# Kernel tuning notes

Measured on AMD Instinct MI355X. Metric: run time of the kernel, lower is better.

## Reference

```python
import jax, jax.numpy as jnp
from jax import lax
import numpy as np

CHI, CHO = 256, 256
B, H, W = 4, 64, 64
KH = KW = 3
K = KH * KW
EPS = 1e-5


def setup_inputs() -> dict:
    key = jax.random.key(0)
    ks = jax.random.split(key, 8)
    x = jax.random.normal(ks[0], (B, CHI, H, W), jnp.float32)
    # offset/mask conv: chi -> 3*K channels (dy[K], dx[K], mask[K]); small init so offsets stay local
    w_off = jax.random.normal(ks[1], (3 * K, CHI, KH, KW), jnp.float32) * 0.01
    b_off = jax.random.normal(ks[2], (3 * K,), jnp.float32) * 0.01
    weight = jax.random.normal(ks[3], (CHO, CHI, KH, KW), jnp.float32) * 0.05
    bias = jax.random.normal(ks[4], (CHO,), jnp.float32) * 0.05
    gamma = 1.0 + 0.1 * jax.random.normal(ks[5], (CHO,), jnp.float32)
    beta = 0.1 * jax.random.normal(ks[6], (CHO,), jnp.float32)
    rmean = 0.1 * jax.random.normal(ks[7], (CHO,), jnp.float32)
    rvar = jnp.ones((CHO,), jnp.float32)
    return {"x": x, "w_off": w_off, "b_off": b_off, "weight": weight,
            "bias": bias, "gamma": gamma, "beta": beta, "rmean": rmean, "rvar": rvar}


def _dcn_bn_relu(x, w_off, b_off, weight, bias, gamma, beta, rmean, rvar):
    Bn, C, Hn, Wn = x.shape
    cho = weight.shape[0]
    # offset/mask branch: ordinary 3x3 same conv
    om = lax.conv_general_dilated(x, w_off, (1, 1), ((1, 1), (1, 1)),
                                  dimension_numbers=("NCHW", "OIHW", "NCHW"))
    om = om + b_off[None, :, None, None]
    o1, o2, m = jnp.split(om, 3, axis=1)            # each [B,K,H,W]
    mask = jax.nn.sigmoid(m).transpose(0, 2, 3, 1)  # [B,H,W,K]
    dy = o1.transpose(0, 2, 3, 1)                   # [B,H,W,K]
    dx = o2.transpose(0, 2, 3, 1)
    # sampling coords: p = out_pos - pad + k*dil + offset (stride=1, pad=1, dil=1)
    ky = jnp.repeat(jnp.arange(KH, dtype=x.dtype) - 1.0, KW)  # [K]
    kx = jnp.tile(jnp.arange(KW, dtype=x.dtype) - 1.0, KH)
    py = jnp.arange(Hn, dtype=x.dtype)[None, :, None, None] + ky + dy  # [B,H,W,K]
    px = jnp.arange(Wn, dtype=x.dtype)[None, None, :, None] + kx + dx

    xt = x.transpose(0, 2, 3, 1)  # [B,H,W,C]
    y0 = jnp.floor(py)
    x0 = jnp.floor(px)
    ly = py - y0
    lx = px - x0
    y0i = y0.astype(jnp.int32)
    x0i = x0.astype(jnp.int32)

    def corner(yi, xi, w):
        valid = (yi >= 0) & (yi < Hn) & (xi >= 0) & (xi < Wn)
        yc = jnp.clip(yi, 0, Hn - 1)
        xc = jnp.clip(xi, 0, Wn - 1)
        v = jax.vmap(lambda img, a, b: img[a, b])(xt, yc, xc)  # [B,H,W,K,C]
        return v * (w * valid.astype(x.dtype))[..., None]

    val = (corner(y0i, x0i, (1 - ly) * (1 - lx))
           + corner(y0i, x0i + 1, (1 - ly) * lx)
           + corner(y0i + 1, x0i, ly * (1 - lx))
           + corner(y0i + 1, x0i + 1, ly * lx))  # [B,H,W,K,C]

    cols = val * mask[..., None]  # modulated columns [B,H,W,K,C]
    wk = weight.reshape(cho, weight.shape[1], K)  # [O,C,K]
    out = jnp.einsum("bhwkc,ock->bohw", cols, wk) + bias[None, :, None, None]
    # BatchNorm (eval: running stats) + ReLU
    inv = gamma * lax.rsqrt(rvar + EPS)
    out = out * inv[None, :, None, None] + (beta - rmean * inv)[None, :, None, None]
    return jax.nn.relu(out)


def reference(x, w_off, b_off, weight, bias, gamma, beta, rmean, rvar):
    return _dcn_bn_relu(x, w_off, b_off, weight, bias, gamma, beta, rmean, rvar)
```

## Files before the change

### kernel.cpp

```cpp
#include <hip/hip_runtime.h>
#include <math.h>

#define NH 64
#define NW 64
#define NB 4
#define CHI 256
#define CHO 256
#define XT_B (8 * 4356 * 32)

#define WREC 40
#define WINSZ (594 * WREC)

typedef __attribute__((ext_vector_type(8))) short bf16x8;
typedef __attribute__((ext_vector_type(4))) float f32x4;

static __device__ __forceinline__ unsigned short f2bf(float f) {
    unsigned int u = __float_as_uint(f);
    u += 0x7fffu + ((u >> 16) & 1u);
    return (unsigned short)(u >> 16);
}
static __device__ __forceinline__ float bflo(unsigned int p) { return __uint_as_float(p << 16); }
static __device__ __forceinline__ float bfhij(unsigned int p) { return __uint_as_float(p); }
static __device__ __forceinline__ unsigned int pkbf(float a, float b) {
    unsigned int r;
    asm("v_cvt_pk_bf16_f32 %0, %1, %2" : "=v"(r) : "v"(a), "v"(b));
    return r;
}

#define BAR_LGKM() asm volatile("s_waitcnt lgkmcnt(0)\n\ts_barrier" ::: "memory")


__global__ __launch_bounds__(256) void prep_all(const float* __restrict__ weight,
                                                const float* __restrict__ w_off,
                                                const float* __restrict__ x,
                                                unsigned short* __restrict__ wB,
                                                unsigned short* __restrict__ wOB,
                                                unsigned short* __restrict__ xT) {
    __shared__ unsigned short sT[64 * 134];
    int bid = blockIdx.x, tid = threadIdx.x;
    if (bid < 576) {
        int idx4 = bid * 256 + tid;
        float4 v = ((const float4*)weight)[idx4];
        float vv[4] = {v.x, v.y, v.z, v.w};
        int i0 = idx4 * 4;
#pragma unroll
        for (int j = 0; j < 4; ++j) {
            int i = i0 + j;
            int o = i / 2304, r = i - o * 2304;
            int c = r / 9, kt = r - c * 9;
            wB[(((c >> 5) * 9 + kt) * 256 + o) * 32 + (c & 31)] = f2bf(vv[j]);
        }
    } else if (bid < 640) {
        int idx4 = (bid - 576) * 256 + tid;
        if (idx4 < 15552) {
            float4 v = ((const float4*)w_off)[idx4];
            float vv[4] = {v.x, v.y, v.z, v.w};
            int i0 = idx4 * 4;
#pragma unroll
            for (int j = 0; j < 4; ++j) {
                int i = i0 + j;
                int oc = i / 2304, r = i - oc * 2304;
                int c = r / 9, kt = r - c * 9;
                wOB[(((c >> 5) * 9 + kt) * 32 + oc) * 32 + (c & 31)] = f2bf(vv[j]);
            }
        }
    } else if (bid == 640) {
        for (int k = tid; k < 11520; k += 256) {
            int ks = k / 160, r = k - ks * 160;
            int oc = 27 + r / 32, kin = r & 31;
            wOB[(ks * 32 + oc) * 32 + kin] = 0;
        }
    } else if (bid < 1153) {
        int bid2 = bid - 641;
        int b = bid2 >> 7, rem = bid2 & 127;
        int y = rem >> 1, chalf = rem & 1;
        int c0 = chalf * 128;
        for (int rep = 0; rep < 8; ++rep) {
            int idx = rep * 256 + tid;
            int c = idx >> 4, p4 = (idx & 15) * 4;
            const float* src = x + (((size_t)b * CHI + c0 + c) * 64 + y) * 64 + p4;
            float4 v = *(const float4*)src;
            sT[(p4 + 0) * 134 + c] = f2bf(v.x);
            sT[(p4 + 1) * 134 + c] = f2bf(v.y);
            sT[(p4 + 2) * 134 + c] = f2bf(v.z);
            sT[(p4 + 3) * 134 + c] = f2bf(v.w);
        }
        __syncthreads();
        unsigned int* xtu = (unsigned int*)xT;
        for (int rep = 0; rep < 4; ++rep) {
            int idx = rep * 256 + tid;
            int px = idx >> 4, cc_l = (idx >> 2) & 3, q4 = idx & 3;
            int cc = chalf * 4 + cc_l;
            int cb = cc_l * 32 + q4 * 8;
            const unsigned int* sp = (const unsigned int*)&sT[px * 134 + cb];
            uint4 vv;
            vv.x = sp[0]; vv.y = sp[1]; vv.z = sp[2]; vv.w = sp[3];
            *(uint4*)&xtu[((size_t)(b * 8 + cc) * 4356
                           + (size_t)(y + 1) * 66 + (px + 1)) * 16 + q4 * 4] = vv;
        }
    } else {
        int flat = (bid - 1153) * 256 + tid;
        int b = flat / 33280, r = flat - b * 33280;
        int chunk = r / 4160, rr = r - chunk * 4160;
        int p_ = rr >> 4, ku = rr & 15;
        int pos;
        if (p_ < 66)       pos = p_;
        else if (p_ < 132) pos = 65 * 66 + (p_ - 66);
        else { int qq = p_ - 132; int side = qq & 1; int row = 1 + (qq >> 1);
               pos = row * 66 + (side ? 65 : 0); }
        unsigned int* xtu = (unsigned int*)xT;
        xtu[((size_t)(b * 8 + chunk) * 4356 + pos) * 16 + ku] = 0;
    }
}

__global__ __launch_bounds__(512, 2) void dcn_fused(
        const unsigned short* __restrict__ xT,
        const unsigned short* __restrict__ wOB,
        const unsigned short* __restrict__ wB,
        const float* __restrict__ b_off,
        const float* __restrict__ bias, const float* __restrict__ gamma,
        const float* __restrict__ beta, const float* __restrict__ rmean,
        const float* __restrict__ rvar, float* __restrict__ out) {
    __shared__ __align__(16) unsigned char smem[154432];
    int4*   s_po = (int4*)smem;
    float4* s_cw = (float4*)(smem + 9216);
    unsigned short* sA = (unsigned short*)(smem + 18432);
    unsigned short* sWin = (unsigned short*)(smem + 59392);
    float* sOff = (float*)(smem + 59392);
    float (*sOut)[260] = (float(*)[260])(smem + 59392);

    int id = blockIdx.x;
    int xcd = id & 7, sl = id >> 3;
    int b = xcd >> 1;
    int h = (xcd & 1) * 32 + sl;

    int tid = threadIdx.x;
    int lane = tid & 63, q = tid >> 6;
    int ln = lane & 15, lk = lane >> 4;
    int nb = q & 3, kh = q >> 2;

    const unsigned short* xTfull = xT + (size_t)b * XT_B;
    const bf16x8* wOBv = (const bf16x8*)wOB;
    const bf16x8* wBv  = (const bf16x8*)wB;

    {
        int omt = q & 1, okq = q >> 1;
        int px0 = omt * 32 + ln;
        int posb = (h + 1) * 66 + 1 + px0;
        f32x4 oa00 = {0.f,0.f,0.f,0.f}, oa01 = {0.f,0.f,0.f,0.f};
        f32x4 oa10 = {0.f,0.f,0.f,0.f}, oa11 = {0.f,0.f,0.f,0.f};
        for (int cc = okq * 2; cc < okq * 2 + 2; ++cc) {
#pragma unroll
            for (int kt = 0; kt < 9; ++kt) {
                int pos = posb + (kt / 3 - 1) * 66 + (kt % 3 - 1);
                bf16x8 A0 = *(const bf16x8*)&xTfull[((size_t)cc * 4356 + pos) * 32 + lk * 8];
                bf16x8 A1 = *(const bf16x8*)&xTfull[((size_t)cc * 4356 + pos + 16) * 32 + lk * 8];
                bf16x8 B0 = wOBv[((size_t)(cc * 9 + kt) * 32 + ln) * 4 + lk];
                bf16x8 B1 = wOBv[((size_t)(cc * 9 + kt) * 32 + 16 + ln) * 4 + lk];
                oa00 = __builtin_amdgcn_mfma_f32_16x16x32_bf16(A0, B0, oa00, 0, 0, 0);
                oa01 = __builtin_amdgcn_mfma_f32_16x16x32_bf16(A0, B1, oa01, 0, 0, 0);
                oa10 = __builtin_amdgcn_mfma_f32_16x16x32_bf16(A1, B0, oa10, 0, 0, 0);
                oa11 = __builtin_amdgcn_mfma_f32_16x16x32_bf16(A1, B1, oa11, 0, 0, 0);
            }
        }
#pragma unroll
        for (int r = 0; r < 4; ++r) {
            int row0 = okq * 64 + omt * 32 + lk * 4 + r;
            sOff[row0 * 33 + ln]            = oa00[r];
            sOff[row0 * 33 + 16 + ln]       = oa01[r];
            sOff[(row0 + 16) * 33 + ln]     = oa10[r];
            sOff[(row0 + 16) * 33 + 16 + ln]= oa11[r];
        }
    }
    BAR_LGKM();

    for (int p = tid; p < 576; p += 512) {
        int k = p >> 6, pwl = p & 63;
        float dy = b_off[k], dx = b_off[k + 9], mp = b_off[k + 18];
#pragma unroll
        for (int jq = 0; jq < 4; ++jq) {
            dy += sOff[(jq * 64 + pwl) * 33 + k];
            dx += sOff[(jq * 64 + pwl) * 33 + k + 9];
            mp += sOff[(jq * 64 + pwl) * 33 + k + 18];
        }
        float mv = 1.f / (1.f + __expf(-mp));
        float py  = (float)h   + (float)(k / 3 - 1) + dy;
        float pxf = (float)pwl + (float)(k % 3 - 1) + dx;
        float y0f = floorf(py), x0f = floorf(pxf);
        int y0 = (int)y0f, x0 = (int)x0f;
        float ly = py - y0f, lx = pxf - x0f;
        int y0c = min(max(y0, -1), 64), y1c = min(max(y0 + 1, -1), 64);
        int x0c = min(max(x0, -1), 64), x1c = min(max(x0 + 1, -1), 64);
        int wy0 = min(max(y0c + 4 - h, 0), 8), wy1 = min(max(y1c + 4 - h, 0), 8);
        int rx0 = x0c + 1, rx1 = x1c + 1;
        s_po[p] = make_int4((wy0 * 66 + rx0) * WREC, (wy0 * 66 + rx1) * WREC,
                            (wy1 * 66 + rx0) * WREC, (wy1 * 66 + rx1) * WREC);
        s_cw[p] = make_float4((1.f - ly) * (1.f - lx) * mv, (1.f - ly) * lx * mv,
                              ly * (1.f - lx) * mv,         ly * lx * mv);
    }

    int cg8 = tid & 3, pxl = (tid >> 2) & 63, khp = tid >> 8;

    f32x4 zf = {0.f, 0.f, 0.f, 0.f};
    f32x4 acc[4][4] = {{zf,zf,zf,zf},{zf,zf,zf,zf},{zf,zf,zf,zf},{zf,zf,zf,zf}};

#define STAGE(pp) do { int ccg_ = khp * 4 + (pp);                              \
        unsigned short* wd_ = sWin + khp * WINSZ;                              \
        int t_ = tid & 255;                                                    \
        for (int rr_ = 0; rr_ < 10; ++rr_) {                                   \
            int idx_ = rr_ * 256 + t_;                                         \
            if (idx_ < 2376) {                                                 \
                int wr_ = idx_ / 264, rg_ = idx_ - wr_ * 264;                  \
                int pr_ = rg_ >> 2, g_ = rg_ & 3;                              \
                int gy_ = min(max(h - 3 + wr_, 0), 65);                        \
                const unsigned short* sp_ = xTfull                             \
                    + ((size_t)(ccg_ * 4356 + gy_ * 66) << 5) + rg_ * 8;       \
                *(uint4*)(wd_ + (size_t)(wr_ * 66 + pr_) * WREC + g_ * 8)      \
                    = *(const uint4*)sp_;                                      \
            }                                                                  \
        }                                                                      \
    } while (0)

#define PACK(kt_, buf_) do {                                                   \
        int4 o4_ = s_po[(kt_) * 64 + pxl];                                     \
        const unsigned short* wb_ = sWin + khp * WINSZ + cg8 * 8;              \
        uint4 C00 = *(const uint4*)(wb_ + (size_t)o4_.x);                      \
        uint4 C01 = *(const uint4*)(wb_ + (size_t)o4_.y);                      \
        uint4 C10 = *(const uint4*)(wb_ + (size_t)o4_.z);                      \
        uint4 C11 = *(const uint4*)(wb_ + (size_t)o4_.w);                      \
        float4 w_ = s_cw[(kt_) * 64 + pxl];                                    \
        uint4 pk_;                                                             \
        pk_.x = pkbf(w_.x*bflo(C00.x)+w_.y*bflo(C01.x)+w_.z*bflo(C10.x)+w_.w*bflo(C11.x), \
                     w_.x*bfhij(C00.x)+w_.y*bfhij(C01.x)+w_.z*bfhij(C10.x)+w_.w*bfhij(C11.x)); \
        pk_.y = pkbf(w_.x*bflo(C00.y)+w_.y*bflo(C01.y)+w_.z*bflo(C10.y)+w_.w*bflo(C11.y), \
                     w_.x*bfhij(C00.y)+w_.y*bfhij(C01.y)+w_.z*bfhij(C10.y)+w_.w*bfhij(C11.y)); \
        pk_.z = pkbf(w_.x*bflo(C00.z)+w_.y*bflo(C01.z)+w_.z*bflo(C10.z)+w_.w*bflo(C11.z), \
                     w_.x*bfhij(C00.z)+w_.y*bfhij(C01.z)+w_.z*bfhij(C10.z)+w_.w*bfhij(C11.z)); \
        pk_.w = pkbf(w_.x*bflo(C00.w)+w_.y*bflo(C01.w)+w_.z*bflo(C10.w)+w_.w*bflo(C11.w), \
                     w_.x*bfhij(C00.w)+w_.y*bfhij(C01.w)+w_.z*bfhij(C10.w)+w_.w*bfhij(C11.w)); \
        *(uint4*)&sA[(buf_) * 2560 + pxl * 40 + cg8 * 8] = pk_;                \
    } while (0)

#define CONSUME(slot_, bf_) do {                                               \
        const unsigned short* pA_ = &sA[(slot_) * 2560];                       \
        bf16x8 a0_ = *(const bf16x8*)&pA_[(0 * 16 + ln) * 40 + lk * 8];        \
        bf16x8 a1_ = *(const bf16x8*)&pA_[(1 * 16 + ln) * 40 + lk * 8];        \
        bf16x8 a2_ = *(const bf16x8*)&pA_[(2 * 16 + ln) * 40 + lk * 8];        \
        bf16x8 a3_ = *(const bf16x8*)&pA_[(3 * 16 + ln) * 40 + lk * 8];        \
        _Pragma("unroll")                                                      \
        for (int j_ = 0; j_ < 4; ++j_) {                                       \
            acc[0][j_] = __builtin_amdgcn_mfma_f32_16x16x32_bf16(a0_, bf_[j_], acc[0][j_], 0, 0, 0); \
            acc[1][j_] = __builtin_amdgcn_mfma_f32_16x16x32_bf16(a1_, bf_[j_], acc[1][j_], 0, 0, 0); \
            acc[2][j_] = __builtin_amdgcn_mfma_f32_16x16x32_bf16(a2_, bf_[j_], acc[2][j_], 0, 0, 0); \
            acc[3][j_] = __builtin_amdgcn_mfma_f32_16x16x32_bf16(a3_, bf_[j_], acc[3][j_], 0, 0, 0); \
        }                                                                      \
    } while (0)

#define WLOAD(bf_, sg_) do { int sgl_ = (sg_);                                 \
        _Pragma("unroll")                                                      \
        for (int j_ = 0; j_ < 4; ++j_)                                         \
            bf_[j_] = wBv[((size_t)(kh * 36 + sgl_) * 256 + nb * 64 + j_ * 16 + ln) * 4 + lk]; \
    } while (0)

    BAR_LGKM();

    STAGE(0);
    BAR_LGKM();

    PACK(0, khp * 2 + 0);
    PACK(1, khp * 2 + 1);
    bf16x8 bfE[4], bfO[4];
    WLOAD(bfE, 0);
    WLOAD(bfO, 1);
    BAR_LGKM();

    for (int p = 0; p < 4; ++p) {
        int s0 = p * 9;
#pragma unroll
        for (int k = 0; k < 4; ++k) {
            if (k < 3) {
                int dset = ((k + 1) & 1) * 4;
                PACK(2 * k + 2, dset + khp * 2 + 0);
                PACK(2 * k + 3, dset + khp * 2 + 1);
            } else {
                PACK(8, khp * 2 + 0);
            }
            int base = (k & 1) * 4 + kh * 2;
            CONSUME(base, bfE);
            if (k < 3) WLOAD(bfE, s0 + 2 * k + 2);
            else       WLOAD(bfE, s0 + 8);
            CONSUME(base + 1, bfO);
            if (k < 3) WLOAD(bfO, s0 + 2 * k + 3);
            BAR_LGKM();
        }
        if (p < 3) STAGE(p + 1);
        CONSUME(kh * 2, bfE);
        BAR_LGKM();
        if (p < 3) {
            PACK(0, khp * 2 + 0);
            PACK(1, khp * 2 + 1);
            WLOAD(bfE, s0 + 9);
            WLOAD(bfO, s0 + 10);
            BAR_LGKM();
        }
    }
#undef STAGE
#undef PACK
#undef CONSUME
#undef WLOAD

    if (kh == 1) {
#pragma unroll
        for (int m = 0; m < 4; ++m)
#pragma unroll
            for (int j = 0; j < 4; ++j) {
                int oc = nb * 64 + j * 16 + ln;
#pragma unroll
                for (int r = 0; r < 4; ++r)
                    sOut[m * 16 + lk * 4 + r][oc] = acc[m][j][r];
            }
    }
    __syncthreads();
    if (kh == 0) {
#pragma unroll
        for (int j = 0; j < 4; ++j) {
            int oc = nb * 64 + j * 16 + ln;
            float inv = gamma[oc] * rsqrtf(rvar[oc] + 1e-5f);
            float sh  = beta[oc] - rmean[oc] * inv + bias[oc] * inv;
#pragma unroll
            for (int m = 0; m < 4; ++m) {
                int row = m * 16 + lk * 4;
                float4 rr;
                rr.x = fmaxf((acc[m][j][0] + sOut[row + 0][oc]) * inv + sh, 0.f);
                rr.y = fmaxf((acc[m][j][1] + sOut[row + 1][oc]) * inv + sh, 0.f);
                rr.z = fmaxf((acc[m][j][2] + sOut[row + 2][oc]) * inv + sh, 0.f);
                rr.w = fmaxf((acc[m][j][3] + sOut[row + 3][oc]) * inv + sh, 0.f);
                size_t oi = (((size_t)b * 256 + oc) * 64 + h) * 64 + row;
                *(float4*)(out + oi) = rr;
            }
        }
    }
}

extern "C" void kernel_launch(void* const* d_in, const int* in_sizes, int n_in,
                              void* d_out, int out_size, void* d_ws, size_t ws_size,
                              hipStream_t stream) {
    const float* x      = (const float*)d_in[0];
    const float* w_off  = (const float*)d_in[1];
    const float* b_off  = (const float*)d_in[2];
    const float* weight = (const float*)d_in[3];
    const float* bias   = (const float*)d_in[4];
    const float* gamma  = (const float*)d_in[5];
    const float* beta   = (const float*)d_in[6];
    const float* rmean  = (const float*)d_in[7];
    const float* rvar   = (const float*)d_in[8];
    float* out = (float*)d_out;

    unsigned short* wB  = (unsigned short*)d_ws;
    unsigned short* wOB = wB + 589824;
    unsigned short* xT  = wOB + 73728;

    hipLaunchKernelGGL(prep_all, dim3(1673), dim3(256), 0, stream,
                       weight, w_off, x, wB, wOB, xT);
    hipLaunchKernelGGL(dcn_fused, dim3(256), dim3(512), 0, stream,
                       xT, wOB, wB, b_off, bias, gamma, beta, rmean, rvar, out);
}
```

Baseline: 126.1 us.

## Double block to 1024 threads, splitting output channels and packing across more waves

```diff
diff --git a/kernel.cpp b/kernel.cpp
--- a/kernel.cpp
+++ b/kernel.cpp
@@ -113,7 +113,7 @@
     }
 }
 
-__global__ __launch_bounds__(512, 2) void dcn_fused(
+__global__ __launch_bounds__(1024, 2) void dcn_fused(
         const unsigned short* __restrict__ xT,
         const unsigned short* __restrict__ wOB,
         const unsigned short* __restrict__ wB,
@@ -137,44 +137,38 @@
     int tid = threadIdx.x;
     int lane = tid & 63, q = tid >> 6;
     int ln = lane & 15, lk = lane >> 4;
-    int nb = q & 3, kh = q >> 2;
+    int nb = q & 7, kh = q >> 3;
 
     const unsigned short* xTfull = xT + (size_t)b * XT_B;
     const bf16x8* wOBv = (const bf16x8*)wOB;
     const bf16x8* wBv  = (const bf16x8*)wB;
 
     {
-        int omt = q & 1, okq = q >> 1;
+        int omt = q & 1, ont = (q >> 1) & 1, okq = q >> 2;
         int px0 = omt * 32 + ln;
         int posb = (h + 1) * 66 + 1 + px0;
-        f32x4 oa00 = {0.f,0.f,0.f,0.f}, oa01 = {0.f,0.f,0.f,0.f};
-        f32x4 oa10 = {0.f,0.f,0.f,0.f}, oa11 = {0.f,0.f,0.f,0.f};
+        f32x4 oa0 = {0.f,0.f,0.f,0.f}, oa1 = {0.f,0.f,0.f,0.f};
         for (int cc = okq * 2; cc < okq * 2 + 2; ++cc) {
 #pragma unroll
             for (int kt = 0; kt < 9; ++kt) {
                 int pos = posb + (kt / 3 - 1) * 66 + (kt % 3 - 1);
                 bf16x8 A0 = *(const bf16x8*)&xTfull[((size_t)cc * 4356 + pos) * 32 + lk * 8];
                 bf16x8 A1 = *(const bf16x8*)&xTfull[((size_t)cc * 4356 + pos + 16) * 32 + lk * 8];
-                bf16x8 B0 = wOBv[((size_t)(cc * 9 + kt) * 32 + ln) * 4 + lk];
-                bf16x8 B1 = wOBv[((size_t)(cc * 9 + kt) * 32 + 16 + ln) * 4 + lk];
-                oa00 = __builtin_amdgcn_mfma_f32_16x16x32_bf16(A0, B0, oa00, 0, 0, 0);
-                oa01 = __builtin_amdgcn_mfma_f32_16x16x32_bf16(A0, B1, oa01, 0, 0, 0);
-                oa10 = __builtin_amdgcn_mfma_f32_16x16x32_bf16(A1, B0, oa10, 0, 0, 0);
-                oa11 = __builtin_amdgcn_mfma_f32_16x16x32_bf16(A1, B1, oa11, 0, 0, 0);
+                bf16x8 B0 = wOBv[((size_t)(cc * 9 + kt) * 32 + ont * 16 + ln) * 4 + lk];
+                oa0 = __builtin_amdgcn_mfma_f32_16x16x32_bf16(A0, B0, oa0, 0, 0, 0);
+                oa1 = __builtin_amdgcn_mfma_f32_16x16x32_bf16(A1, B0, oa1, 0, 0, 0);
             }
         }
 #pragma unroll
         for (int r = 0; r < 4; ++r) {
-            int row0 = okq * 64 + omt * 32 + lk * 4 + r;
-            sOff[row0 * 33 + ln]            = oa00[r];
-            sOff[row0 * 33 + 16 + ln]       = oa01[r];
-            sOff[(row0 + 16) * 33 + ln]     = oa10[r];
-            sOff[(row0 + 16) * 33 + 16 + ln]= oa11[r];
+            int row0 = omt * 32 + lk * 4 + r;
+            sOff[(okq * 64 + row0) * 33 + ont * 16 + ln]      = oa0[r];
+            sOff[(okq * 64 + row0 + 16) * 33 + ont * 16 + ln] = oa1[r];
         }
     }
     BAR_LGKM();
 
-    for (int p = tid; p < 576; p += 512) {
+    for (int p = tid; p < 576; p += 1024) {
         int k = p >> 6, pwl = p & 63;
         float dy = b_off[k], dx = b_off[k + 9], mp = b_off[k + 18];
 #pragma unroll
@@ -199,16 +193,17 @@
                               ly * (1.f - lx) * mv,         ly * lx * mv);
     }
 
-    int cg8 = tid & 3, pxl = (tid >> 2) & 63, khp = tid >> 8;
+    int cg8 = tid & 3, pxl = (tid >> 2) & 63;
+    int sl4 = tid >> 8, khp = sl4 >> 1, ip = sl4 & 1;
 
     f32x4 zf = {0.f, 0.f, 0.f, 0.f};
-    f32x4 acc[4][4] = {{zf,zf,zf,zf},{zf,zf,zf,zf},{zf,zf,zf,zf},{zf,zf,zf,zf}};
+    f32x4 acc[4][2] = {{zf,zf},{zf,zf},{zf,zf},{zf,zf}};
 
 #define STAGE(pp) do { int ccg_ = khp * 4 + (pp);                              \
         unsigned short* wd_ = sWin + khp * WINSZ;                              \
-        int t_ = tid & 255;                                                    \
-        for (int rr_ = 0; rr_ < 10; ++rr_) {                                   \
-            int idx_ = rr_ * 256 + t_;                                         \
+        int t_ = tid & 511;                                                    \
+        for (int rr_ = 0; rr_ < 5; ++rr_) {                                    \
+            int idx_ = rr_ * 512 + t_;                                         \
             if (idx_ < 2376) {                                                 \
                 int wr_ = idx_ / 264, rg_ = idx_ - wr_ * 264;                  \
                 int pr_ = rg_ >> 2, g_ = rg_ & 3;                              \
@@ -248,7 +243,7 @@
         bf16x8 a2_ = *(const bf16x8*)&pA_[(2 * 16 + ln) * 40 + lk * 8];        \
         bf16x8 a3_ = *(const bf16x8*)&pA_[(3 * 16 + ln) * 40 + lk * 8];        \
         _Pragma("unroll")                                                      \
-        for (int j_ = 0; j_ < 4; ++j_) {                                       \
+        for (int j_ = 0; j_ < 2; ++j_) {                                       \
             acc[0][j_] = __builtin_amdgcn_mfma_f32_16x16x32_bf16(a0_, bf_[j_], acc[0][j_], 0, 0, 0); \
             acc[1][j_] = __builtin_amdgcn_mfma_f32_16x16x32_bf16(a1_, bf_[j_], acc[1][j_], 0, 0, 0); \
             acc[2][j_] = __builtin_amdgcn_mfma_f32_16x16x32_bf16(a2_, bf_[j_], acc[2][j_], 0, 0, 0); \
@@ -258,8 +253,8 @@
 
 #define WLOAD(bf_, sg_) do { int sgl_ = (sg_);                                 \
         _Pragma("unroll")                                                      \
-        for (int j_ = 0; j_ < 4; ++j_)                                         \
-            bf_[j_] = wBv[((size_t)(kh * 36 + sgl_) * 256 + nb * 64 + j_ * 16 + ln) * 4 + lk]; \
+        for (int j_ = 0; j_ < 2; ++j_)                                         \
+            bf_[j_] = wBv[((size_t)(kh * 36 + sgl_) * 256 + nb * 32 + j_ * 16 + ln) * 4 + lk]; \
     } while (0)
 
     BAR_LGKM();
@@ -267,9 +262,8 @@
     STAGE(0);
     BAR_LGKM();
 
-    PACK(0, khp * 2 + 0);
-    PACK(1, khp * 2 + 1);
-    bf16x8 bfE[4], bfO[4];
+    PACK(ip, khp * 2 + ip);
+    bf16x8 bfE[2], bfO[2];
     WLOAD(bfE, 0);
     WLOAD(bfO, 1);
     BAR_LGKM();
@@ -280,10 +274,9 @@
         for (int k = 0; k < 4; ++k) {
             if (k < 3) {
                 int dset = ((k + 1) & 1) * 4;
-                PACK(2 * k + 2, dset + khp * 2 + 0);
-                PACK(2 * k + 3, dset + khp * 2 + 1);
-            } else {
-                PACK(8, khp * 2 + 0);
+                PACK(2 * k + 2 + ip, dset + khp * 2 + ip);
+            } else if (ip == 0) {
+                PACK(8, khp * 2);
             }
             int base = (k & 1) * 4 + kh * 2;
             CONSUME(base, bfE);
@@ -297,8 +290,7 @@
         CONSUME(kh * 2, bfE);
         BAR_LGKM();
         if (p < 3) {
-            PACK(0, khp * 2 + 0);
-            PACK(1, khp * 2 + 1);
+            PACK(ip, khp * 2 + ip);
             WLOAD(bfE, s0 + 9);
             WLOAD(bfO, s0 + 10);
             BAR_LGKM();
@@ -313,8 +305,8 @@
 #pragma unroll
         for (int m = 0; m < 4; ++m)
 #pragma unroll
-            for (int j = 0; j < 4; ++j) {
-                int oc = nb * 64 + j * 16 + ln;
+            for (int j = 0; j < 2; ++j) {
+                int oc = nb * 32 + j * 16 + ln;
 #pragma unroll
                 for (int r = 0; r < 4; ++r)
                     sOut[m * 16 + lk * 4 + r][oc] = acc[m][j][r];
@@ -323,8 +315,8 @@
     __syncthreads();
     if (kh == 0) {
 #pragma unroll
-        for (int j = 0; j < 4; ++j) {
-            int oc = nb * 64 + j * 16 + ln;
+        for (int j = 0; j < 2; ++j) {
+            int oc = nb * 32 + j * 16 + ln;
             float inv = gamma[oc] * rsqrtf(rvar[oc] + 1e-5f);
             float sh  = beta[oc] - rmean[oc] * inv + bias[oc] * inv;
 #pragma unroll
@@ -362,6 +354,6 @@
 
     hipLaunchKernelGGL(prep_all, dim3(1673), dim3(256), 0, stream,
                        weight, w_off, x, wB, wOB, xT);
-    hipLaunchKernelGGL(dcn_fused, dim3(256), dim3(512), 0, stream,
+    hipLaunchKernelGGL(dcn_fused, dim3(256), dim3(1024), 0, stream,
                        xT, wOB, wB, b_off, bias, gamma, beta, rmean, rvar, out);
 }
```

New measurement: 129.8 us. 3.0% more time.
